# Optimization experiments

Measured on AMD Instinct MI355X. Metric: run time of the kernel, lower is better.

Reference implementation:

```python
import jax, jax.numpy as jnp
import numpy as np

K = 3
KK = K * K
EPS = 1e-5


def conv2d(x, w, b, pad):
    y = jax.lax.conv_general_dilated(x, w, (1, 1), [(pad, pad), (pad, pad)],
                                     dimension_numbers=("NCHW", "OIHW", "NCHW"))
    return y + b[None, :, None, None]


def bn(x, g, b, m, v):
    inv = g / jnp.sqrt(v + EPS)
    return x * inv[None, :, None, None] + (b - m * inv)[None, :, None, None]


def deform_sample(x, dy, dx):
    # x: [B,C,H,W]; dy,dx: [B,KK,H,W] -> sampled [B,C,KK,H,W] (bilinear, zeros outside)
    B, C, H, W = x.shape
    k = jnp.arange(K, dtype=x.dtype) - 1.0  # pad=1, dilation=1, stride=1
    ky = jnp.repeat(k, K)  # [KK] row offsets
    kx = jnp.tile(k, K)    # [KK] col offsets
    hh = jnp.arange(H, dtype=x.dtype)
    ww = jnp.arange(W, dtype=x.dtype)
    py = hh[None, :, None] + ky[:, None, None] + dy  # [B,KK,H,W]
    px = ww[None, None, :] + kx[:, None, None] + dx

    def sample_one(img, py, px):
        y0f = jnp.floor(py); x0f = jnp.floor(px)
        wy = py - y0f; wx = px - x0f
        y0 = y0f.astype(jnp.int32); x0 = x0f.astype(jnp.int32)

        def gather(yi, xi, w):
            valid = (yi >= 0) & (yi < H) & (xi >= 0) & (xi < W)
            yc = jnp.clip(yi, 0, H - 1); xc = jnp.clip(xi, 0, W - 1)
            v = img[:, yc, xc]  # [C,KK,H,W]
            return v * (w * valid)[None]

        return (gather(y0, x0, (1 - wy) * (1 - wx)) +
                gather(y0, x0 + 1, (1 - wy) * wx) +
                gather(y0 + 1, x0, wy * (1 - wx)) +
                gather(y0 + 1, x0 + 1, wy * wx))

    return jax.vmap(sample_one)(x, py, px)


def setup_inputs() -> dict:
    key = jax.random.key(0)
    ks = jax.random.split(key, 16)
    B, C, H, W = 8, 256, 64, 64
    d = {
        "feature": jax.random.normal(ks[0], (B, C, H, W), jnp.float32),
        "p1_w": jax.random.normal(ks[1], (C, C, 1, 1), jnp.float32) * 0.05,
        "p1_b": jax.random.normal(ks[2], (C,), jnp.float32) * 0.05,
        "bn1_g": jax.random.normal(ks[3], (C,), jnp.float32) * 0.1 + 1.0,
        "bn1_b": jax.random.normal(ks[4], (C,), jnp.float32) * 0.05,
        "bn1_m": jax.random.normal(ks[5], (C,), jnp.float32) * 0.05,
        "bn1_v": jax.random.uniform(ks[6], (C,), jnp.float32) + 0.5,
        "off_w": jax.random.normal(ks[7], (3 * KK, 2 * C, K, K), jnp.float32) * 0.01,
        "off_b": jax.random.normal(ks[8], (3 * KK,), jnp.float32) * 0.01,
        "dcn_w": jax.random.normal(ks[9], (C, C, K, K), jnp.float32) * 0.05,
        "dcn_b": jax.random.normal(ks[10], (C,), jnp.float32) * 0.05,
        "bn2_g": jax.random.normal(ks[11], (C,), jnp.float32) * 0.1 + 1.0,
        "bn2_b": jax.random.normal(ks[12], (C,), jnp.float32) * 0.05,
        "bn2_m": jax.random.normal(ks[13], (C,), jnp.float32) * 0.05,
        "bn2_v": jax.random.uniform(ks[14], (C,), jnp.float32) + 0.5,
    }
    return d


def reference(feature, p1_w, p1_b, bn1_g, bn1_b, bn1_m, bn1_v,
              off_w, off_b, dcn_w, dcn_b, bn2_g, bn2_b, bn2_m, bn2_v):
    flipped = feature[..., ::-1]                      # flip last (W) axis
    proj = bn(conv2d(feature, p1_w, p1_b, 0), bn1_g, bn1_b, bn1_m, bn1_v)
    # DCNv2: offsets/mask from concat(flipped, proj)
    concat = jnp.concatenate([flipped, proj], axis=1)
    off = conv2d(concat, off_w, off_b, 1)             # [B,27,H,W]
    dy = off[:, :KK]
    dx = off[:, KK:2 * KK]
    mask = jax.nn.sigmoid(off[:, 2 * KK:])            # [B,KK,H,W]
    sampled = deform_sample(flipped, dy, dx)          # [B,C,KK,H,W]
    O = dcn_w.shape[0]
    y = jnp.einsum("bckhw,ock->bohw", sampled * mask[:, None], dcn_w.reshape(O, -1, KK))
    y = y + dcn_b[None, :, None, None]
    y = bn(y, bn2_g, bn2_b, bn2_m, bn2_v)
    return jax.nn.relu(proj + y)
```

## Files before the change

kernel.cpp:

```cpp
#include <hip/hip_runtime.h>
#include <hip/hip_bf16.h>
#include <math.h>

typedef __attribute__((ext_vector_type(8))) short short8;
typedef __attribute__((ext_vector_type(4))) short short4v;
typedef __attribute__((ext_vector_type(4))) float f32x4;
typedef __attribute__((ext_vector_type(2))) float f32x2;

__device__ __forceinline__ float bs2f(short s){
    union { unsigned u; float f; } x; x.u = ((unsigned)(unsigned short)s) << 16; return x.f;
}
__device__ __forceinline__ short f2bs(float f){
    union { float f; unsigned u; } x; x.f = f;
    unsigned r = x.u + 0x7fff + ((x.u >> 16) & 1);
    return (short)(r >> 16);
}
__device__ __forceinline__ f32x2 up2(unsigned u){
    union { unsigned u; float f; } lo, hi;
    lo.u = u << 16; hi.u = u & 0xffff0000u;
    f32x2 r; r.x = lo.f; r.y = hi.f; return r;
}
__device__ __forceinline__ unsigned pk2rn(float lo, float hi){
    __hip_bfloat162 h = __float22bfloat162_rn(make_float2(lo, hi));
    union { __hip_bfloat162 h; unsigned u; } cv; cv.h = h; return cv.u;
}
__device__ __forceinline__ void gl2lds16(const void* g, void* l){
    __builtin_amdgcn_global_load_lds(
        (const __attribute__((address_space(1))) void*)g,
        (__attribute__((address_space(3))) void*)l, 16, 0, 0);
}
__device__ __forceinline__ void hard_barrier(){
    __builtin_amdgcn_sched_barrier(0);
    __builtin_amdgcn_s_barrier();
    __builtin_amdgcn_sched_barrier(0);
}
__device__ __forceinline__ void lds_barrier(){
    __builtin_amdgcn_sched_barrier(0);
    asm volatile("s_waitcnt lgkmcnt(0)" ::: "memory");
    __builtin_amdgcn_s_barrier();
    __builtin_amdgcn_sched_barrier(0);
}

#define XPB ((size_t)66*66*512)


__global__ void k_prep(const float* __restrict__ p1_w, const float* __restrict__ p1_b,
                       const float* __restrict__ bn1_g, const float* __restrict__ bn1_b,
                       const float* __restrict__ bn1_m, const float* __restrict__ bn1_v,
                       const float* __restrict__ off_w,
                       const float* __restrict__ dcn_w, const float* __restrict__ dcn_b,
                       const float* __restrict__ bn2_g, const float* __restrict__ bn2_b,
                       const float* __restrict__ bn2_m, const float* __restrict__ bn2_v,
                       short* __restrict__ p1_wb, short* __restrict__ Wofrag,
                       short* __restrict__ Wfrag,
                       float* __restrict__ bias1f, float* __restrict__ inv2f,
                       float* __restrict__ bias2f, unsigned* __restrict__ XpadU)
{
    int blk = blockIdx.x, t = threadIdx.x;
    if (blk == 0) {
        float inv1 = bn1_g[t] / sqrtf(bn1_v[t] + 1e-5f);
        bias1f[t] = p1_b[t] * inv1 + bn1_b[t] - bn1_m[t] * inv1;
        float inv2 = bn2_g[t] / sqrtf(bn2_v[t] + 1e-5f);
        inv2f[t] = inv2;
        bias2f[t] = dcn_b[t] * inv2 + bn2_b[t] - bn2_m[t] * inv2;
    } else if (blk <= 256) {
        int o = blk - 1;
        float inv1 = bn1_g[o] / sqrtf(bn1_v[o] + 1e-5f);
        p1_wb[o*256 + t] = f2bs(p1_w[o*256 + t] * inv1);
    } else if (blk <= 512) {
        int o = blk - 257;
        const float* src = dcn_w + (size_t)o*2304;
        uint4* dst = (uint4*)Wfrag;
        int strip = o >> 4, lnn = o & 15;
        #pragma unroll
        for (int r = 0; r < 2; ++r) {
            int j = r*256 + t;
            if (j < 288) {
                int tap = j >> 5, c0 = (j & 31) * 8;
                union { short s[8]; uint4 u; } v;
                #pragma unroll
                for (int e = 0; e < 8; ++e)
                    v.s[e] = f2bs(src[(c0 + e)*9 + tap]);
                dst[(size_t)((j >> 2)*16 + strip)*64 + (j & 3)*16 + lnn] = v.u;
            }
        }
    } else if (blk <= 584) {
        int gidx = (blk - 513)*256 + t;
        int kc = gidx >> 7;
        int rem = gidx & 127;
        int strip = rem >> 6, lane2 = rem & 63;
        int ln2 = lane2 & 15, q2 = lane2 >> 4;
        int row = strip*16 + ln2;
        union { short s[8]; uint4 u; } v;
        #pragma unroll
        for (int e = 0; e < 8; ++e) {
            int k = kc*32 + q2*8 + e;
            int tap = k >> 9, ci = k & 511;
            v.s[e] = (row < 27) ? f2bs(off_w[(size_t)row*4608 + ci*9 + tap]) : (short)0;
        }
        ((uint4*)Wofrag)[gidx] = v.u;
    } else {
        int hb = blk - 585;
        int b = hb / 260, i = hb % 260;
        int y, x;
        if (i < 66)       { y = 0;  x = i; }
        else if (i < 132) { y = 65; x = i - 66; }
        else { int j = i - 132; y = 1 + (j >> 1); x = (j & 1) * 65; }
        XpadU[((size_t)(b*66 + y)*66 + x)*256 + t] = 0u;
    }
}

__global__ __launch_bounds__(512, 2) void k_fproj(
    const float* __restrict__ feature, short* Xpad,
    const short* __restrict__ p1_wb, const float* __restrict__ bias1f)
{
    __shared__ __align__(16) unsigned char sh_u[16640];
    __shared__ __align__(16) short Bt[8][2048];
    float (*tile)[65] = (float(*)[65])sh_u;
    short* Ash = (short*)sh_u;
    int bid = blockIdx.x;
    int b = bid & 7, h = bid >> 3;
    int t = threadIdx.x;
    int lane = t & 63, w = t >> 6;
    int lw = t & 63, li = t >> 6;
    int ln = lane & 15, q = lane >> 4;
    int r16 = lane >> 2;
    int sq  = (lane & 3) ^ ((lane >> 3) & 3);
    int rq  = (q ^ ((ln >> 1) & 3)) * 8;
    size_t rowbase = (size_t)(b*66 + h + 1)*66;

    for (int cg = 0; cg < 4; ++cg) {
        int c0 = cg * 64;
        #pragma unroll
        for (int j = 0; j < 8; ++j) {
            int cl = j*8 + li;
            tile[cl][63 - lw] = feature[((b*256 + c0 + cl)*64 + h)*64 + lw];
        }
        __syncthreads();
        #pragma unroll
        for (int j = 0; j < 8; ++j) {
            int x = j*8 + li;
            short s  = f2bs(tile[lw][x]);
            Xpad[(rowbase + x + 1)*512 + c0 + lw] = s;
            short sB = f2bs(tile[lw][63 - x]);
            int c = c0 + lw;
            int kt = c >> 5, kk = c & 31, p = kk >> 3, e = kk & 7;
            Bt[kt][x*32 + ((p ^ ((x >> 1) & 3)) << 3) + e] = sB;
        }
        __syncthreads();
    }

    f32x4 acc[2][4] = {};
    for (int kt = 0; kt < 8; ++kt) {
        int kcol = kt*32 + sq*8;
        #pragma unroll
        for (int i = 0; i < 2; ++i) {
            int row = w*32 + i*16 + r16;
            gl2lds16(p1_wb + (size_t)row*256 + kcol, Ash + (w*32 + i*16)*32);
        }
        __syncthreads();
        short8 af[2], bfr[4];
        #pragma unroll
        for (int i = 0; i < 2; ++i)
            af[i] = *(const short8*)&Ash[(w*32 + i*16 + ln)*32 + rq];
        #pragma unroll
        for (int j = 0; j < 4; ++j)
            bfr[j] = *(const short8*)&Bt[kt][(j*16 + ln)*32 + rq];
        #pragma unroll
        for (int i = 0; i < 2; ++i)
            #pragma unroll
            for (int j = 0; j < 4; ++j)
                acc[i][j] = __builtin_amdgcn_mfma_f32_16x16x32_bf16(af[i], bfr[j], acc[i][j], 0, 0, 0);
        __syncthreads();
    }
    #pragma unroll
    for (int i = 0; i < 2; ++i) {
        int ob = w*32 + i*16 + q*4;
        #pragma unroll
        for (int j = 0; j < 4; ++j) {
            int x = j*16 + ln;
            size_t xb = (rowbase + x + 1)*512 + 256 + ob;
            short4v st;
            st.x = f2bs(acc[i][j][0] + bias1f[ob]);
            st.y = f2bs(acc[i][j][1] + bias1f[ob+1]);
            st.z = f2bs(acc[i][j][2] + bias1f[ob+2]);
            st.w = f2bs(acc[i][j][3] + bias1f[ob+3]);
            *(short4v*)&Xpad[xb] = st;
        }
    }
}

__global__ __launch_bounds__(512, 4) void k_offm(
    const short* __restrict__ Xpad, const uint4* __restrict__ Wof4,
    const float* __restrict__ off_b, float* __restrict__ offv)
{
    __shared__ short Bsh[8][64*32];
    int bid = blockIdx.x;
    int b = bid & 7, h = bid >> 3;
    int t = threadIdx.x;
    int lane = t & 63, w = t >> 6;
    int ln = lane & 15, q = lane >> 4;
    int wr = w >> 2, wc = w & 3;
    int r16 = lane >> 2;
    int sq  = (lane & 3) ^ ((lane >> 3) & 3);
    int rq  = (q ^ ((ln >> 1) & 3)) * 8;
    const short* xb = Xpad + (size_t)b*XPB;

    f32x4 acc = {};
    for (int it = 0; it < 18; ++it) {
        int tap = it >> 1;
        int dy = tap/3 - 1, dx = tap%3 - 1;
        uint4 a[8];
        #pragma unroll
        for (int s = 0; s < 8; ++s)
            a[s] = Wof4[(size_t)((it*8 + s)*2 + wr)*64 + lane];
        {
            int k = it*256 + w*32;
            #pragma unroll
            for (int g = 0; g < 4; ++g) {
                int row = g*16 + r16;
                const short* gB = xb + ((size_t)(h + 1 + dy)*66 + (row + dx + 1))*512
                                     + (k & 511) + sq*8;
                gl2lds16(gB, &Bsh[w][(g*16)*32]);
            }
        }
        __syncthreads();
        #pragma unroll
        for (int s = 0; s < 8; ++s) {
            short8 af  = *(short8*)&a[s];
            short8 bfr = *(const short8*)&Bsh[s][(wc*16 + ln)*32 + rq];
            acc = __builtin_amdgcn_mfma_f32_16x16x32_bf16(af, bfr, acc, 0, 0, 0);
        }
        __syncthreads();
    }
    int x = wc*16 + ln;
    #pragma unroll
    for (int r = 0; r < 4; ++r) {
        int oc = wr*16 + q*4 + r;
        if (oc < 27)
            offv[((b*27 + oc)*64 + h)*64 + x] = acc[r] + off_b[oc];
    }
}

#define ALOAD4(kn_, A_)                                                   \
    A_##0 = Wf4[(size_t)(((kn_)*2+0)*16 + tw0)*64 + lane];                \
    A_##1 = Wf4[(size_t)(((kn_)*2+0)*16 + tw1)*64 + lane];                \
    A_##2 = Wf4[(size_t)(((kn_)*2+1)*16 + tw0)*64 + lane];                \
    A_##3 = Wf4[(size_t)(((kn_)*2+1)*16 + tw1)*64 + lane];

#define MMPHASE(A_)                                                       \
    {                                                                     \
        short8 af00 = *(short8*)&A_##0, af01 = *(short8*)&A_##1;          \
        short8 af10 = *(short8*)&A_##2, af11 = *(short8*)&A_##3;          \
        short8 bfr;                                                       \
        _Pragma("unroll")                                                 \
        for (int jj = 0; jj < 4; ++jj) {                                  \
            bfr = *(const short8*)&Bsh[0][(jj*16 + ln)*32 + rq];          \
            acc[0][jj] = __builtin_amdgcn_mfma_f32_16x16x32_bf16(af00, bfr, acc[0][jj], 0, 0, 0); \
            acc[1][jj] = __builtin_amdgcn_mfma_f32_16x16x32_bf16(af01, bfr, acc[1][jj], 0, 0, 0); \
        }                                                                 \
        _Pragma("unroll")                                                 \
        for (int jj = 0; jj < 4; ++jj) {                                  \
            bfr = *(const short8*)&Bsh[1][(jj*16 + ln)*32 + rq];          \
            acc[0][jj] = __builtin_amdgcn_mfma_f32_16x16x32_bf16(af10, bfr, acc[0][jj], 0, 0, 0); \
            acc[1][jj] = __builtin_amdgcn_mfma_f32_16x16x32_bf16(af11, bfr, acc[1][jj], 0, 0, 0); \
        }                                                                 \
    }

#define WINX(kc2_, AC_, AN_, UC_, VN_)                                    \
    {                                                                     \
        int kn_ = (kc2_) < 35 ? (kc2_) + 1 : 35;                          \
        ALOAD4(kn_, AN_);                                                 \
        GATHER(kn_, VN_);                                                 \
        __builtin_amdgcn_sched_barrier(0);                                \
        BLEND(UC_, (kc2_) >> 2);                                          \
        lds_barrier();                                                    \
        MMPHASE(AC_);                                                     \
        hard_barrier();                                                   \
    }

__global__ __launch_bounds__(512, 3) void k_gemm(
    const short* __restrict__ Xpad,
    const short* __restrict__ Wfrag,
    const float* __restrict__ offv,
    const float* __restrict__ inv2f, const float* __restrict__ bias2f,
    float* __restrict__ out)
{
    __shared__ __align__(16) short Bsh[2][64*32];
    __shared__ unsigned c_pk[576];
    __shared__ float c_w[576*4];
    int bid = blockIdx.x;
    int b = bid & 7, h = bid >> 3;
    int t = threadIdx.x;
    int lane = t & 63, w = t >> 6;
    int ln = lane & 15, q = lane >> 4;
    int rq  = (q ^ ((ln >> 1) & 3)) * 8;
    int tw0 = w*2, tw1 = w*2 + 1;
    const uint4* Wf4 = (const uint4*)Wfrag;

    for (int e = t; e < 576; e += 512) {
        int p = e / 9, k = e % 9;
        int base = (b*27)*4096 + h*64 + p;
        float dy = offv[base + k*4096];
        float dx = offv[base + (9+k)*4096];
        float ms = offv[base + (18+k)*4096];
        ms = 1.f / (1.f + expf(-ms));
        float py = (float)h + (float)(k/3 - 1) + dy;
        float px = (float)p + (float)(k%3 - 1) + dx;
        float y0f = floorf(py), x0f = floorf(px);
        float wy = py - y0f, wx = px - x0f;
        int y0 = (int)y0f, x0 = (int)x0f;
        int y1 = y0 + 1, x1 = x0 + 1;
        float vy0 = (y0 >= 0 && y0 < 64) ? 1.f : 0.f;
        float vy1 = (y1 >= 0 && y1 < 64) ? 1.f : 0.f;
        float vx0 = (x0 >= 0 && x0 < 64) ? 1.f : 0.f;
        float vx1 = (x1 >= 0 && x1 < 64) ? 1.f : 0.f;
        int y0c = min(max(y0,0),63), y1c = min(max(y1,0),63);
        int x0c = min(max(x0,0),63), x1c = min(max(x1,0),63);
        unsigned cell = (unsigned)(((y0c+1)*66 + x0c+1)*128);
        unsigned sx = (x1c != x0c) ? 1u : 0u;
        unsigned sy = (y1c != y0c) ? 1u : 0u;
        c_pk[e] = cell | (sx << 20) | (sy << 21);
        c_w[e*4+0] = ms * (1.f-wy)*(1.f-wx) * vy0*vx0;
        c_w[e*4+1] = ms * (1.f-wy)*wx       * vy0*vx1;
        c_w[e*4+2] = ms * wy*(1.f-wx)       * vy1*vx0;
        c_w[e*4+3] = ms * wy*wx             * vy1*vx1;
    }
    __syncthreads();

    const uint2* fT = (const uint2*)Xpad + (size_t)b*(XPB/4);
    int pr = t >> 3;
    int jo = t & 7;
    int pe9 = pr*9;
    short* bdst = &Bsh[jo >> 2][pr*32 + (((jo & 3) ^ ((pr >> 1) & 3)) << 3)];

    f32x4 acc[2][4] = {};
    uint4 U[4], V[4];
    uint4 a00, a01, a02, a03;
    uint4 a10, a11, a12, a13;

    auto GATHER = [&](int win, uint4 (&dst)[4]) {
        unsigned pw = c_pk[pe9 + (win >> 2)];
        int o00 = pw & 0xFFFFF;
        int dxs = (pw >> 13) & 128;
        int dys = ((pw >> 8) & 0x2000) | ((pw >> 13) & 0x100);
        int cin = ((win & 3) << 4) + jo*2;
        const uint2* p0 = fT + (o00 + cin);
        dst[0] = *(const uint4*)(p0);
        dst[1] = *(const uint4*)(p0 + dxs);
        dst[2] = *(const uint4*)(p0 + dys);
        dst[3] = *(const uint4*)(p0 + dys + dxs);
    };
    auto BLEND = [&](uint4 (&uc)[4], int tap) {
        const float4 cw = *(const float4*)&c_w[(pe9 + tap)*4];
        f32x2 Wx; Wx.x = cw.x; Wx.y = cw.x;
        f32x2 Wy; Wy.x = cw.y; Wy.y = cw.y;
        f32x2 Wz; Wz.x = cw.z; Wz.y = cw.z;
        f32x2 Ww; Ww.x = cw.w; Ww.y = cw.w;
        f32x2 G0 = Wx*up2(uc[0].x) + Wy*up2(uc[1].x) + Wz*up2(uc[2].x) + Ww*up2(uc[3].x);
        f32x2 G1 = Wx*up2(uc[0].y) + Wy*up2(uc[1].y) + Wz*up2(uc[2].y) + Ww*up2(uc[3].y);
        f32x2 G2 = Wx*up2(uc[0].z) + Wy*up2(uc[1].z) + Wz*up2(uc[2].z) + Ww*up2(uc[3].z);
        f32x2 G3 = Wx*up2(uc[0].w) + Wy*up2(uc[1].w) + Wz*up2(uc[2].w) + Ww*up2(uc[3].w);
        uint4 pkv;
        pkv.x = pk2rn(G0.x, G0.y);
        pkv.y = pk2rn(G1.x, G1.y);
        pkv.z = pk2rn(G2.x, G2.y);
        pkv.w = pk2rn(G3.x, G3.y);
        *(uint4*)bdst = pkv;
    };

    ALOAD4(0, a0);
    GATHER(0, U);
    __builtin_amdgcn_sched_barrier(0);
    #pragma unroll 1
    for (int kc2 = 0; kc2 < 36; kc2 += 2) {
        WINX(kc2,     a0, a1, U, V);
        WINX(kc2 + 1, a1, a0, V, U);
    }

    #pragma unroll
    for (int i = 0; i < 2; ++i) {
        int ob = w*32 + i*16 + q*4;
        #pragma unroll
        for (int jj = 0; jj < 4; ++jj) {
            int p = jj*16 + ln;
            size_t xb = ((size_t)(b*66 + h + 1)*66 + p + 1)*512 + 256 + ob;
            short4v prr = *(const short4v*)&Xpad[xb];
            #pragma unroll
            for (int r = 0; r < 4; ++r) {
                int o = ob + r;
                size_t idx = ((size_t)(b*256 + o))*4096 + h*64 + p;
                float rs = bs2f(((const short*)&prr)[r]);
                float v = rs + acc[i][jj][r]*inv2f[o] + bias2f[o];
                out[idx] = v < 0.f ? 0.f : v;
            }
        }
    }
}

extern "C" void kernel_launch(void* const* d_in, const int* in_sizes, int n_in,
                              void* d_out, int out_size, void* d_ws, size_t ws_size,
                              hipStream_t stream)
{
    const float* feature = (const float*)d_in[0];
    const float* p1_w  = (const float*)d_in[1];
    const float* p1_b  = (const float*)d_in[2];
    const float* bn1_g = (const float*)d_in[3];
    const float* bn1_b = (const float*)d_in[4];
    const float* bn1_m = (const float*)d_in[5];
    const float* bn1_v = (const float*)d_in[6];
    const float* off_w = (const float*)d_in[7];
    const float* off_b = (const float*)d_in[8];
    const float* dcn_w = (const float*)d_in[9];
    const float* dcn_b = (const float*)d_in[10];
    const float* bn2_g = (const float*)d_in[11];
    const float* bn2_b = (const float*)d_in[12];
    const float* bn2_m = (const float*)d_in[13];
    const float* bn2_v = (const float*)d_in[14];

    float* ws = (float*)d_ws;
    short* Xpad   = (short*)ws;
    float* offbuf = ws + 8921088;
    short* p1_wb  = (short*)(ws + 9805824);
    short* Wofrag = (short*)(ws + 9838592);
    short* Wfrag  = (short*)(ws + 9912320);
    float* bias1f = ws + 10207232;
    float* inv2f  = ws + 10207488;
    float* bias2f = ws + 10207744;

    k_prep<<<2665, 256, 0, stream>>>(p1_w, p1_b, bn1_g, bn1_b, bn1_m, bn1_v,
                                     off_w, dcn_w, dcn_b, bn2_g, bn2_b, bn2_m, bn2_v,
                                     p1_wb, Wofrag, Wfrag, bias1f, inv2f, bias2f,
                                     (unsigned*)Xpad);
    k_fproj<<<512, 512, 0, stream>>>(feature, Xpad, p1_wb, bias1f);
    k_offm<<<512, 512, 0, stream>>>(Xpad, (const uint4*)Wofrag, off_b, offbuf);
    k_gemm<<<512, 512, 0, stream>>>(Xpad, Wfrag, offbuf, inv2f, bias2f, (float*)d_out);
}
```

Baseline: 222.6 us.

## Fuse offset/mask conv into deformable GEMM kernel via shared memory

```diff
diff --git a/kernel.cpp b/kernel.cpp
--- a/kernel.cpp
+++ b/kernel.cpp
@@ -190,58 +190,6 @@
     }
 }
 
-__global__ __launch_bounds__(512, 4) void k_offm(
-    const short* __restrict__ Xpad, const uint4* __restrict__ Wof4,
-    const float* __restrict__ off_b, float* __restrict__ offv)
-{
-    __shared__ short Bsh[8][64*32];
-    int bid = blockIdx.x;
-    int b = bid & 7, h = bid >> 3;
-    int t = threadIdx.x;
-    int lane = t & 63, w = t >> 6;
-    int ln = lane & 15, q = lane >> 4;
-    int wr = w >> 2, wc = w & 3;
-    int r16 = lane >> 2;
-    int sq  = (lane & 3) ^ ((lane >> 3) & 3);
-    int rq  = (q ^ ((ln >> 1) & 3)) * 8;
-    const short* xb = Xpad + (size_t)b*XPB;
-
-    f32x4 acc = {};
-    for (int it = 0; it < 18; ++it) {
-        int tap = it >> 1;
-        int dy = tap/3 - 1, dx = tap%3 - 1;
-        uint4 a[8];
-        #pragma unroll
-        for (int s = 0; s < 8; ++s)
-            a[s] = Wof4[(size_t)((it*8 + s)*2 + wr)*64 + lane];
-        {
-            int k = it*256 + w*32;
-            #pragma unroll
-            for (int g = 0; g < 4; ++g) {
-                int row = g*16 + r16;
-                const short* gB = xb + ((size_t)(h + 1 + dy)*66 + (row + dx + 1))*512
-                                     + (k & 511) + sq*8;
-                gl2lds16(gB, &Bsh[w][(g*16)*32]);
-            }
-        }
-        __syncthreads();
-        #pragma unroll
-        for (int s = 0; s < 8; ++s) {
-            short8 af  = *(short8*)&a[s];
-            short8 bfr = *(const short8*)&Bsh[s][(wc*16 + ln)*32 + rq];
-            acc = __builtin_amdgcn_mfma_f32_16x16x32_bf16(af, bfr, acc, 0, 0, 0);
-        }
-        __syncthreads();
-    }
-    int x = wc*16 + ln;
-    #pragma unroll
-    for (int r = 0; r < 4; ++r) {
-        int oc = wr*16 + q*4 + r;
-        if (oc < 27)
-            offv[((b*27 + oc)*64 + h)*64 + x] = acc[r] + off_b[oc];
-    }
-}
-
 #define ALOAD4(kn_, A_)                                                   \
     A_##0 = Wf4[(size_t)(((kn_)*2+0)*16 + tw0)*64 + lane];                \
     A_##1 = Wf4[(size_t)(((kn_)*2+0)*16 + tw1)*64 + lane];                \
@@ -279,13 +227,16 @@
         hard_barrier();                                                   \
     }
 
-__global__ __launch_bounds__(512, 3) void k_gemm(
+__global__ __launch_bounds__(512, 4) void k_gemm(
     const short* __restrict__ Xpad,
     const short* __restrict__ Wfrag,
-    const float* __restrict__ offv,
+    const uint4* __restrict__ Wof4,
+    const float* __restrict__ off_b,
     const float* __restrict__ inv2f, const float* __restrict__ bias2f,
     float* __restrict__ out)
 {
+    __shared__ __align__(16) short BshO[8][64*32];
+    __shared__ float red[27][65];
     __shared__ __align__(16) short Bsh[2][64*32];
     __shared__ unsigned c_pk[576];
     __shared__ float c_w[576*4];
@@ -298,12 +249,53 @@
     int tw0 = w*2, tw1 = w*2 + 1;
     const uint4* Wf4 = (const uint4*)Wfrag;
 
+    {
+        int wr = w >> 2, wc = w & 3;
+        int r16 = lane >> 2;
+        int sq  = (lane & 3) ^ ((lane >> 3) & 3);
+        const short* xb = Xpad + (size_t)b*XPB;
+        f32x4 oacc = {};
+        for (int it = 0; it < 18; ++it) {
+            int tap = it >> 1;
+            int dy = tap/3 - 1, dx = tap%3 - 1;
+            uint4 a[8];
+            #pragma unroll
+            for (int s = 0; s < 8; ++s)
+                a[s] = Wof4[(size_t)((it*8 + s)*2 + wr)*64 + lane];
+            {
+                int k = it*256 + w*32;
+                #pragma unroll
+                for (int g = 0; g < 4; ++g) {
+                    int row = g*16 + r16;
+                    const short* gB = xb + ((size_t)(h + 1 + dy)*66 + (row + dx + 1))*512
+                                         + (k & 511) + sq*8;
+                    gl2lds16(gB, &BshO[w][(g*16)*32]);
+                }
+            }
+            __syncthreads();
+            #pragma unroll
+            for (int s = 0; s < 8; ++s) {
+                short8 af  = *(short8*)&a[s];
+                short8 bfr = *(const short8*)&BshO[s][(wc*16 + ln)*32 + rq];
+                oacc = __builtin_amdgcn_mfma_f32_16x16x32_bf16(af, bfr, oacc, 0, 0, 0);
+            }
+            __syncthreads();
+        }
+        int x = wc*16 + ln;
+        #pragma unroll
+        for (int r = 0; r < 4; ++r) {
+            int oc = wr*16 + q*4 + r;
+            if (oc < 27)
+                red[oc][x] = oacc[r] + off_b[oc];
+        }
+    }
+    __syncthreads();
+
     for (int e = t; e < 576; e += 512) {
         int p = e / 9, k = e % 9;
-        int base = (b*27)*4096 + h*64 + p;
-        float dy = offv[base + k*4096];
-        float dx = offv[base + (9+k)*4096];
-        float ms = offv[base + (18+k)*4096];
+        float dy = red[k][p];
+        float dx = red[9+k][p];
+        float ms = red[18+k][p];
         ms = 1.f / (1.f + expf(-ms));
         float py = (float)h + (float)(k/3 - 1) + dy;
         float px = (float)p + (float)(k%3 - 1) + dx;
@@ -420,7 +412,6 @@
 
     float* ws = (float*)d_ws;
     short* Xpad   = (short*)ws;
-    float* offbuf = ws + 8921088;
     short* p1_wb  = (short*)(ws + 9805824);
     short* Wofrag = (short*)(ws + 9838592);
     short* Wfrag  = (short*)(ws + 9912320);
@@ -433,6 +424,6 @@
                                      p1_wb, Wofrag, Wfrag, bias1f, inv2f, bias2f,
                                      (unsigned*)Xpad);
     k_fproj<<<512, 512, 0, stream>>>(feature, Xpad, p1_wb, bias1f);
-    k_offm<<<512, 512, 0, stream>>>(Xpad, (const uint4*)Wofrag, off_b, offbuf);
-    k_gemm<<<512, 512, 0, stream>>>(Xpad, Wfrag, offbuf, inv2f, bias2f, (float*)d_out);
-}
+    k_gemm<<<512, 512, 0, stream>>>(Xpad, Wfrag, (const uint4*)Wofrag, off_b,
+                                    inv2f, bias2f, (float*)d_out);
+}
```

After: 215.2 us. 3.3% less time.
